# Performance work log

Hardware: AMD Instinct MI355X
Metric: run time of the kernel (lower is better)

Reference implementation:

```python
import jax, jax.numpy as jnp
import numpy as np

N = 100000   # nodes
E = 1600000  # edges (avg degree 16)
DIM = 3      # coordinate dims
R = 3        # pseudo-coordinate dim
C = 32       # channels / Gaussian kernels
F = 64       # non-coordinate node features


def setup_inputs() -> dict:
    key = jax.random.key(0)
    k1, k2, k3, k4, k5 = jax.random.split(key, 5)
    features = jax.random.normal(k1, (N, DIM + F), dtype=jnp.float32)
    edge_index = jax.random.randint(k2, (E, 2), 0, N, dtype=jnp.int32)  # (row=i, col=j) per edge
    w_dense = jax.random.normal(k3, (DIM, R), dtype=jnp.float32) / jnp.sqrt(jnp.float32(DIM))  # lecun-ish
    b_dense = jnp.zeros((R,), dtype=jnp.float32)
    mu = jax.random.normal(k4, (C, N, R), dtype=jnp.float32) * 0.1
    # sigma initialized positive (abs of lecun normal in the original); keep bounded away from 0
    sig = jax.random.uniform(k5, (C, N, R), dtype=jnp.float32, minval=0.1, maxval=1.0)
    return {"features": features, "edge_index": edge_index,
            "w_dense": w_dense, "b_dense": b_dense, "mu": mu, "sig": sig}


def reference(features, edge_index, w_dense, b_dense, mu, sig):
    coords = features[:, :DIM]          # [N, 3]
    h = features[:, DIM:]               # [N, F]
    src = edge_index[:, 0]              # row index i per edge
    dst = edge_index[:, 1]              # col index j per edge
    # per-edge pseudo-coordinates: tanh(Dense_r(x_j - x_i))
    u = jnp.tanh((coords[dst] - coords[src]) @ w_dense + b_dense)      # [E, R]
    # Gaussian-mixture edge weight per (channel, edge), mu/sigma gathered at row node i
    diff = u[None, :, :] - mu[:, src, :]                               # [C, E, R]
    w = jnp.exp(-0.5 * jnp.sum(diff * diff / sig[:, src, :], axis=-1)) # [C, E]
    # (A o W) @ H summed over feature axis == sum_j w[c,i,j] * sum_f H[j,f]
    msg = w * jnp.sum(h, axis=-1)[dst][None, :]                        # [C, E]
    agg = jax.ops.segment_sum(msg.T, src, num_segments=N)              # [N, C]
    return jnp.concatenate([coords, agg], axis=-1)                     # [N, DIM + C]
```

## Files before the change

### kernel.cpp

```cpp
#include <hip/hip_runtime.h>

#define DIMV 3
#define RV 3
#define CV 32
#define ROWF 67
#define ROWO 35
#define CAP 48
#define PADSTR 49
#define SCAN_T 1024
#define NGRP 8
#define BSH 5
#define BNODES 32
#define SEGCAP 192

__device__ __forceinline__ float fast_tanh(float x) {
    float ex = __expf(2.0f * x);
    return (ex - 1.0f) * __builtin_amdgcn_rcpf(ex + 1.0f);
}

__device__ __forceinline__ int xcc_id() {
    int x;
    asm("s_getreg_b32 %0, hwreg(HW_REG_XCC_ID)" : "=s"(x));
    return x & (NGRP - 1);
}

__global__ void prep_kernel(const float* __restrict__ features,
                            float4* __restrict__ nd,
                            int* __restrict__ counts,
                            int* __restrict__ bcur, int nbc,
                            float* __restrict__ out, int N) {
    int gid = blockIdx.x * blockDim.x + threadIdx.x;
    if (gid < N) counts[gid] = 0;
    if (gid < nbc) bcur[gid] = 0;
    int node = gid >> 6;
    int lane = threadIdx.x & 63;
    if (node >= N) return;
    const float* row = features + (size_t)node * ROWF;
    float f0 = row[lane];
    float f1 = (lane < ROWF - 64) ? row[64 + lane] : 0.0f;
    float v = (lane >= DIMV ? f0 : 0.0f) + f1;
    for (int off = 32; off > 0; off >>= 1) v += __shfl_xor(v, off, 64);
    float c0 = __shfl(f0, 0, 64);
    float c1 = __shfl(f0, 1, 64);
    float c2 = __shfl(f0, 2, 64);
    if (lane == 0) nd[node] = make_float4(c0, c1, c2, v);
    if (lane < DIMV) out[(size_t)node * ROWO + lane] = f0;
}

__global__ void bin_kernel(const int2* __restrict__ ei2,
                           int* __restrict__ bcur,
                           unsigned int* __restrict__ bins, int E, int NB) {
    int grp = xcc_id();
    int stride = gridDim.x * blockDim.x;
    for (int e = blockIdx.x * blockDim.x + threadIdx.x; e < E; e += stride) {
        unsigned long long v =
            __builtin_nontemporal_load((const unsigned long long*)ei2 + e);
        int s = (int)(v & 0xffffffffull);
        int d = (int)(v >> 32);
        int b = s >> BSH;
        int g = grp;
        int slot = atomicAdd(bcur + g * NB + b, 1);
#pragma unroll 1
        for (int tries = 0; slot >= SEGCAP && tries < NGRP; ++tries) {
            g = (g + 1) & (NGRP - 1);
            slot = atomicAdd(bcur + g * NB + b, 1);
        }
        if (slot < SEGCAP)
            bins[(size_t)(g * NB + b) * SEGCAP + slot] =
                ((unsigned)(s & (BNODES - 1)) << 17) | (unsigned)d;
    }
}

__global__ __launch_bounds__(256, 6)
void fused_bucket_kernel(const int* __restrict__ bcur,
                         const unsigned int* __restrict__ bins,
                         const float4* __restrict__ nd,
                         const float* __restrict__ wd,
                         const float* __restrict__ bd,
                         const float* __restrict__ mu,
                         const float* __restrict__ sig,
                         float* __restrict__ out, int N, int NB) {
    __shared__ float4 ue[BNODES * PADSTR];
    __shared__ float4 snd[BNODES];
    __shared__ int lcnt[BNODES];
    __shared__ int soff[NGRP + 1];
    int b = blockIdx.x;
    int base = b << BSH;
    int nn = N - base; if (nn > BNODES) nn = BNODES;
    int t = threadIdx.x;
    if (t < BNODES) {
        lcnt[t] = 0;
        snd[t] = (t < nn) ? nd[base + t] : make_float4(0.f, 0.f, 0.f, 0.f);
    }
    if (t < NGRP) {
        int c = bcur[t * NB + b];
        soff[t + 1] = (c > SEGCAP) ? SEGCAP : c;
    }
    if (t == 0) soff[0] = 0;
    __syncthreads();
    if (t == 0) {
#pragma unroll
        for (int g = 0; g < NGRP; ++g) soff[g + 1] += soff[g];
    }
    __syncthreads();
    {
        float w0 = wd[0], w1 = wd[1], w2 = wd[2];
        float w3 = wd[3], w4 = wd[4], w5 = wd[5];
        float w6 = wd[6], w7 = wd[7], w8 = wd[8];
        float b0 = bd[0], b1 = bd[1], b2 = bd[2];
        int total = soff[NGRP];
        for (int r = t; r < total; r += 256) {
            int g = 0;
#pragma unroll
            for (int gg = 1; gg < NGRP; ++gg) if (r >= soff[gg]) g = gg;
            int i = r - soff[g];
            unsigned p = bins[(size_t)(g * NB + b) * SEGCAP + i];
            int sl = p >> 17;
            int d  = p & 0x1FFFF;
            float4 pd = nd[d];
            int k = atomicAdd(&lcnt[sl], 1);
            if (k >= CAP) k = CAP - 1;
            float4 ps = snd[sl];
            float dx = pd.x - ps.x, dy = pd.y - ps.y, dz = pd.z - ps.z;
            float u0 = fast_tanh(dx * w0 + dy * w3 + dz * w6 + b0);
            float u1 = fast_tanh(dx * w1 + dy * w4 + dz * w7 + b1);
            float u2 = fast_tanh(dx * w2 + dy * w5 + dz * w8 + b2);
            ue[sl * PADSTR + (k ^ ((sl >> 3) & 3))] = make_float4(u0, u1, u2, pd.w);
        }
    }
    __syncthreads();
    int wv = t >> 6;
    int l  = t & 63;
    int h  = l >> 5;
    int n  = l & 31;
    size_t slab = (size_t)N * RV;
    int nid = base + ((n < nn) ? n : 0);
    float3 mv[4], sv[4];
#pragma unroll
    for (int j = 0; j < 4; ++j) {
        int c = 8 * wv + 2 * j + h;
        const float* mp = mu  + (size_t)c * slab + (size_t)nid * RV;
        const float* sp = sig + (size_t)c * slab + (size_t)nid * RV;
        mv[j] = *(const float3*)mp;
        sv[j] = *(const float3*)sp;
    }
    float mm[4][3], im[4][3], acc[4];
#pragma unroll
    for (int j = 0; j < 4; ++j) {
        mm[j][0] = mv[j].x; mm[j][1] = mv[j].y; mm[j][2] = mv[j].z;
        im[j][0] = __builtin_amdgcn_rcpf(sv[j].x);
        im[j][1] = __builtin_amdgcn_rcpf(sv[j].y);
        im[j][2] = __builtin_amdgcn_rcpf(sv[j].z);
        acc[j] = 0.0f;
    }
    int cnt = (n < nn) ? min(lcnt[n], CAP) : 0;
    int key = (n >> 3) & 3;
    for (int k = 0; k < cnt; ++k) {
        float4 q = ue[n * PADSTR + (k ^ key)];
#pragma unroll
        for (int j = 0; j < 4; ++j) {
            float d0 = q.x - mm[j][0], d1 = q.y - mm[j][1], d2 = q.z - mm[j][2];
            float t2 = d0 * d0 * im[j][0] + d1 * d1 * im[j][1] + d2 * d2 * im[j][2];
            acc[j] += __expf(-0.5f * t2) * q.w;
        }
    }
    if (n < nn) {
        float* orow = out + (size_t)(base + n) * ROWO + DIMV;
#pragma unroll
        for (int j = 0; j < 4; ++j) orow[8 * wv + 2 * j + h] = acc[j];
    }
}


__global__ void hist_kernel(const int2* __restrict__ ei2, int* __restrict__ counts, int E) {
    int e = blockIdx.x * blockDim.x + threadIdx.x;
    if (e >= E) return;
    atomicAdd(counts + ei2[e].x, 1);
}

__global__ void scan_a_kernel(const int* __restrict__ counts, int* __restrict__ offsets,
                              int* __restrict__ partials, int N) {
    __shared__ int sm[SCAN_T];
    int t = threadIdx.x;
    int i = blockIdx.x * SCAN_T + t;
    int c = (i < N) ? counts[i] : 0;
    sm[t] = c;
    __syncthreads();
    for (int off = 1; off < SCAN_T; off <<= 1) {
        int v = (t >= off) ? sm[t - off] : 0;
        __syncthreads();
        sm[t] += v;
        __syncthreads();
    }
    if (i < N) offsets[i] = sm[t] - c;
    if (t == SCAN_T - 1) partials[blockIdx.x] = sm[t];
}

__global__ void scan_b_kernel(int* __restrict__ partials, int B) {
    __shared__ int sm[SCAN_T];
    int t = threadIdx.x;
    int c = (t < B) ? partials[t] : 0;
    sm[t] = c;
    __syncthreads();
    for (int off = 1; off < SCAN_T; off <<= 1) {
        int v = (t >= off) ? sm[t - off] : 0;
        __syncthreads();
        sm[t] += v;
        __syncthreads();
    }
    if (t < B) partials[t] = sm[t] - c;
}

__global__ void scan_c_kernel(int* __restrict__ offsets, const int* __restrict__ partials,
                              int* __restrict__ cursor, int N, int E) {
    int i = blockIdx.x * blockDim.x + threadIdx.x;
    if (i == 0) offsets[N] = E;
    if (i >= N) return;
    int off = offsets[i] + partials[i / SCAN_T];
    offsets[i] = off;
    cursor[i] = off;
}

__global__ void scatter_u_kernel(const int2* __restrict__ ei2, int* __restrict__ cursor,
                                 const float4* __restrict__ nd,
                                 const float* __restrict__ wd, const float* __restrict__ bd,
                                 float4* __restrict__ ue, int E) {
    int e = blockIdx.x * blockDim.x + threadIdx.x;
    if (e >= E) return;
    int2 sd = ei2[e];
    int pos = atomicAdd(cursor + sd.x, 1);
    float4 ps = nd[sd.x];
    float4 pd = nd[sd.y];
    float dx = pd.x - ps.x, dy = pd.y - ps.y, dz = pd.z - ps.z;
    float u0 = fast_tanh(dx * wd[0] + dy * wd[3] + dz * wd[6] + bd[0]);
    float u1 = fast_tanh(dx * wd[1] + dy * wd[4] + dz * wd[7] + bd[1]);
    float u2 = fast_tanh(dx * wd[2] + dy * wd[5] + dz * wd[8] + bd[2]);
    ue[pos] = make_float4(u0, u1, u2, pd.w);
}

__global__ void node_acc2_kernel(const int* __restrict__ offsets,
                                 const float4* __restrict__ ue,
                                 const float* __restrict__ mu,
                                 const float* __restrict__ sig,
                                 float* __restrict__ out, int N) {
    int node = (blockIdx.x * blockDim.x + threadIdx.x) >> 6;
    if (node >= N) return;
    int lane = threadIdx.x & 63;
    int c = lane & 31;
    int half = lane >> 5;
    size_t slab = (size_t)N * RV;
    const float* mp = mu + (size_t)c * slab + (size_t)node * RV;
    const float* sp = sig + (size_t)c * slab + (size_t)node * RV;
    float m0 = mp[0], m1 = mp[1], m2 = mp[2];
    float i0 = __builtin_amdgcn_rcpf(sp[0]);
    float i1 = __builtin_amdgcn_rcpf(sp[1]);
    float i2 = __builtin_amdgcn_rcpf(sp[2]);
    int off0 = offsets[node], off1 = offsets[node + 1];
    float acc = 0.0f;
    for (int i = off0 + half; i < off1; i += 2) {
        float4 q = ue[i];
        float d0 = q.x - m0, d1 = q.y - m1, d2 = q.z - m2;
        float t = d0 * d0 * i0 + d1 * d1 * i1 + d2 * d2 * i2;
        acc += __expf(-0.5f * t) * q.w;
    }
    acc += __shfl_xor(acc, 32, 64);
    if (half == 0) out[(size_t)node * ROWO + DIMV + c] = acc;
}


__global__ void fb_pre_kernel(const float* __restrict__ features,
                              float4* __restrict__ nd, float* __restrict__ out, int N) {
    int gid = blockIdx.x * blockDim.x + threadIdx.x;
    int node = gid >> 6;
    int lane = threadIdx.x & 63;
    if (node >= N) return;
    const float* row = features + (size_t)node * ROWF;
    float f0 = row[lane];
    float f1 = (lane < ROWF - 64) ? row[64 + lane] : 0.0f;
    float v = (lane >= DIMV ? f0 : 0.0f) + f1;
    for (int off = 32; off > 0; off >>= 1) v += __shfl_xor(v, off, 64);
    float c0 = __shfl(f0, 0, 64);
    float c1 = __shfl(f0, 1, 64);
    float c2 = __shfl(f0, 2, 64);
    if (lane == 0) nd[node] = make_float4(c0, c1, c2, v);
    float* orow = out + (size_t)node * ROWO;
    if (lane < DIMV) orow[lane] = f0;
    else if (lane < ROWO) orow[lane] = 0.0f;
}

__global__ void fb_edge_kernel(const int* __restrict__ ei, const float4* __restrict__ nd,
                               const float* __restrict__ wd, const float* __restrict__ bd,
                               const float* __restrict__ mu, const float* __restrict__ sig,
                               float* __restrict__ out, int N, int E) {
    int e = blockIdx.x * blockDim.x + threadIdx.x;
    if (e >= E) return;
    int s = ei[2 * e];
    int d = ei[2 * e + 1];
    float4 ps = nd[s];
    float4 pd = nd[d];
    float dx = pd.x - ps.x, dy = pd.y - ps.y, dz = pd.z - ps.z;
    float u0 = fast_tanh(dx * wd[0] + dy * wd[3] + dz * wd[6] + bd[0]);
    float u1 = fast_tanh(dx * wd[1] + dy * wd[4] + dz * wd[7] + bd[1]);
    float u2 = fast_tanh(dx * wd[2] + dy * wd[5] + dz * wd[8] + bd[2]);
    float hs = pd.w;
    float* oagg = out + (size_t)s * ROWO + DIMV;
    size_t nodeoff = (size_t)s * RV;
    size_t slab = (size_t)N * RV;
#pragma unroll 4
    for (int c = 0; c < CV; ++c) {
        const float* mp = mu + (size_t)c * slab + nodeoff;
        const float* sp = sig + (size_t)c * slab + nodeoff;
        float d0 = u0 - mp[0], d1 = u1 - mp[1], d2 = u2 - mp[2];
        float t = d0 * d0 * __builtin_amdgcn_rcpf(sp[0])
                + d1 * d1 * __builtin_amdgcn_rcpf(sp[1])
                + d2 * d2 * __builtin_amdgcn_rcpf(sp[2]);
        atomicAdd(oagg + c, __expf(-0.5f * t) * hs);
    }
}

extern "C" void kernel_launch(void* const* d_in, const int* in_sizes, int n_in,
                              void* d_out, int out_size, void* d_ws, size_t ws_size,
                              hipStream_t stream) {
    const float* features = (const float*)d_in[0];
    const int*   ei       = (const int*)d_in[1];
    const int2*  ei2      = (const int2*)d_in[1];
    const float* wd       = (const float*)d_in[2];
    const float* bd       = (const float*)d_in[3];
    const float* mu       = (const float*)d_in[4];
    const float* sig      = (const float*)d_in[5];
    float* out = (float*)d_out;

    int N = in_sizes[0] / ROWF;
    int E = in_sizes[1] / 2;
    int B = (N + SCAN_T - 1) / SCAN_T;
    int NB = (N + BNODES - 1) / BNODES;

    size_t cur = 0;
    auto take = [&](size_t bytes) { size_t p = cur; cur += (bytes + 255) & ~(size_t)255; return p; };
    size_t o_nd      = take((size_t)N * sizeof(float4));
    size_t o_counts  = take((size_t)N * sizeof(int));
    size_t o_offsets = take((size_t)(N + 1) * sizeof(int));
    size_t o_cursor  = take((size_t)N * sizeof(int));
    size_t o_part    = take((size_t)SCAN_T * sizeof(int));
    size_t o_bcur    = take((size_t)NGRP * NB * sizeof(int));
    size_t o_bins    = take((size_t)NGRP * NB * SEGCAP * sizeof(unsigned int));
    size_t o_tail    = cur;
    size_t need_fused = o_tail;
    size_t need_full  = o_tail + (((size_t)E * sizeof(float4) + 255) & ~(size_t)255);

    char* ws = (char*)d_ws;
    float4* nd   = (float4*)(ws + o_nd);
    int* counts  = (int*)(ws + o_counts);
    int* offsets = (int*)(ws + o_offsets);
    int* cursor  = (int*)(ws + o_cursor);
    int* part    = (int*)(ws + o_part);
    int* bcur    = (int*)(ws + o_bcur);
    unsigned int* bins = (unsigned int*)(ws + o_bins);

    if (ws_size >= need_fused && N < (1 << 17)) {
        prep_kernel<<<(N + 3) / 4, 256, 0, stream>>>(features, nd, counts, bcur, NGRP * NB, out, N);
        bin_kernel<<<2048, 256, 0, stream>>>(ei2, bcur, bins, E, NB);
        fused_bucket_kernel<<<NB, 256, 0, stream>>>(bcur, bins, nd, wd, bd, mu, sig, out, N, NB);
    } else if (ws_size >= need_full && B <= SCAN_T) {
        float4* ue = (float4*)(ws + o_tail);
        prep_kernel<<<(N + 3) / 4, 256, 0, stream>>>(features, nd, counts, bcur, 0, out, N);
        hist_kernel<<<(E + 255) / 256, 256, 0, stream>>>(ei2, counts, E);
        scan_a_kernel<<<B, SCAN_T, 0, stream>>>(counts, offsets, part, N);
        scan_b_kernel<<<1, SCAN_T, 0, stream>>>(part, B);
        scan_c_kernel<<<(N + 255) / 256, 256, 0, stream>>>(offsets, part, cursor, N, E);
        scatter_u_kernel<<<(E + 255) / 256, 256, 0, stream>>>(ei2, cursor, nd, wd, bd, ue, E);
        node_acc2_kernel<<<(N + 3) / 4, 256, 0, stream>>>(offsets, ue, mu, sig, out, N);
    } else {
        fb_pre_kernel<<<(N + 3) / 4, 256, 0, stream>>>(features, nd, out, N);
        fb_edge_kernel<<<(E + 255) / 256, 256, 0, stream>>>(ei, nd, wd, bd, mu, sig, out, N, E);
    }
}
```

Before: 256.8 us.

## Replace per-bucket global-atomic binning with LDS-staged coarse partition binning

Edges are now binned into coarse partitions of 1024 source nodes. Each large block stages records in per-partition LDS ring buffers and flushes them in 16-record chunks, using one global atomic per chunk instead of one per edge. Each 32-node bucket block then scans its whole partition with vectorized loads and keeps only the records for its own node group. This cuts global atomic traffic and scattered writes, but every bucket block now reads about 32x more records (mostly from L2) and does a divergent filter. The LDS ring can also overwrite entries if more than 64 edges for one partition arrive in a single pass.

```diff
diff --git a/kernel.cpp b/kernel.cpp
--- a/kernel.cpp
+++ b/kernel.cpp
@@ -8,20 +8,19 @@
 #define CAP 48
 #define PADSTR 49
 #define SCAN_T 1024
-#define NGRP 8
 #define BSH 5
 #define BNODES 32
-#define SEGCAP 192
+#define PART_SH 10
+#define MAXP 128
+#define RING 64
+#define PSEG 24576
+#define CB_BLOCKS 256
+#define CB_THREADS 1024
+#define INVALID_REC 0xFFFFFFFFu
 
 __device__ __forceinline__ float fast_tanh(float x) {
     float ex = __expf(2.0f * x);
     return (ex - 1.0f) * __builtin_amdgcn_rcpf(ex + 1.0f);
-}
-
-__device__ __forceinline__ int xcc_id() {
-    int x;
-    asm("s_getreg_b32 %0, hwreg(HW_REG_XCC_ID)" : "=s"(x));
-    return x & (NGRP - 1);
 }
 
 __global__ void prep_kernel(const float* __restrict__ features,
@@ -47,60 +46,92 @@
     if (lane < DIMV) out[(size_t)node * ROWO + lane] = f0;
 }
 
-__global__ void bin_kernel(const int2* __restrict__ ei2,
-                           int* __restrict__ bcur,
-                           unsigned int* __restrict__ bins, int E, int NB) {
-    int grp = xcc_id();
-    int stride = gridDim.x * blockDim.x;
-    for (int e = blockIdx.x * blockDim.x + threadIdx.x; e < E; e += stride) {
-        unsigned long long v =
-            __builtin_nontemporal_load((const unsigned long long*)ei2 + e);
-        int s = (int)(v & 0xffffffffull);
-        int d = (int)(v >> 32);
-        int b = s >> BSH;
-        int g = grp;
-        int slot = atomicAdd(bcur + g * NB + b, 1);
-#pragma unroll 1
-        for (int tries = 0; slot >= SEGCAP && tries < NGRP; ++tries) {
-            g = (g + 1) & (NGRP - 1);
-            slot = atomicAdd(bcur + g * NB + b, 1);
+__global__ __launch_bounds__(CB_THREADS, 1)
+void coarse_bin_kernel(const int2* __restrict__ ei2,
+                       int* __restrict__ gcur,
+                       unsigned int* __restrict__ bins, int E, int P) {
+    __shared__ unsigned int ring[MAXP][RING];
+    __shared__ int cnt[MAXP];
+    __shared__ int flushed[MAXP];
+    int t = threadIdx.x;
+    for (int i = t; i < P; i += CB_THREADS) { cnt[i] = 0; flushed[i] = 0; }
+    __syncthreads();
+    long long e0 = (long long)E * blockIdx.x / CB_BLOCKS;
+    long long e1 = (long long)E * (blockIdx.x + 1) / CB_BLOCKS;
+    int wv = t >> 6, lane = t & 63;
+    for (long long cs = e0; cs < e1; cs += 2 * CB_THREADS) {
+#pragma unroll
+        for (int j = 0; j < 2; ++j) {
+            long long e = cs + (long long)j * CB_THREADS + t;
+            if (e < e1) {
+                unsigned long long v =
+                    __builtin_nontemporal_load((const unsigned long long*)ei2 + e);
+                int s = (int)(v & 0xffffffffull);
+                int d = (int)(v >> 32);
+                int p = s >> PART_SH;
+                int slot = atomicAdd(&cnt[p], 1);
+                ring[p][slot & (RING - 1)] =
+                    ((unsigned)(s & ((1 << PART_SH) - 1)) << 17) | (unsigned)d;
+            }
         }
-        if (slot < SEGCAP)
-            bins[(size_t)(g * NB + b) * SEGCAP + slot] =
-                ((unsigned)(s & (BNODES - 1)) << 17) | (unsigned)d;
+        __syncthreads();
+        for (int p2 = wv; p2 < P; p2 += CB_THREADS / 64) {
+            int c = cnt[p2];
+            int fl = flushed[p2];
+            int pend = (c >> 4) - fl;
+            while (pend > 0) {
+                int L = pend > 4 ? 4 : pend;
+                int gpos = 0;
+                if (lane == 0) gpos = atomicAdd(&gcur[p2], L << 4);
+                gpos = __shfl(gpos, 0, 64);
+                if (lane < (L << 4) && gpos + (L << 4) <= PSEG)
+                    bins[(size_t)p2 * PSEG + gpos + lane] =
+                        ring[p2][((fl << 4) + lane) & (RING - 1)];
+                fl += L;
+                pend -= L;
+            }
+            if (lane == 0) flushed[p2] = fl;
+        }
+        __syncthreads();
+    }
+    for (int p2 = wv; p2 < P; p2 += CB_THREADS / 64) {
+        int c = cnt[p2];
+        int fl = flushed[p2];
+        int rem = c - (fl << 4);
+        if (rem > 0) {
+            int gpos = 0;
+            if (lane == 0) gpos = atomicAdd(&gcur[p2], 16);
+            gpos = __shfl(gpos, 0, 64);
+            if (lane < 16 && gpos + 16 <= PSEG) {
+                unsigned r = (lane < rem)
+                    ? ring[p2][((fl << 4) + lane) & (RING - 1)] : INVALID_REC;
+                bins[(size_t)p2 * PSEG + gpos + lane] = r;
+            }
+        }
     }
 }
 
 __global__ __launch_bounds__(256, 6)
-void fused_bucket_kernel(const int* __restrict__ bcur,
+void fused_bucket_kernel(const int* __restrict__ gcur,
                          const unsigned int* __restrict__ bins,
                          const float4* __restrict__ nd,
                          const float* __restrict__ wd,
                          const float* __restrict__ bd,
                          const float* __restrict__ mu,
                          const float* __restrict__ sig,
-                         float* __restrict__ out, int N, int NB) {
+                         float* __restrict__ out, int N) {
     __shared__ float4 ue[BNODES * PADSTR];
     __shared__ float4 snd[BNODES];
     __shared__ int lcnt[BNODES];
-    __shared__ int soff[NGRP + 1];
     int b = blockIdx.x;
     int base = b << BSH;
     int nn = N - base; if (nn > BNODES) nn = BNODES;
     int t = threadIdx.x;
+    int p   = b >> (PART_SH - BSH);
+    int grp = b & ((1 << (PART_SH - BSH)) - 1);
     if (t < BNODES) {
         lcnt[t] = 0;
         snd[t] = (t < nn) ? nd[base + t] : make_float4(0.f, 0.f, 0.f, 0.f);
-    }
-    if (t < NGRP) {
-        int c = bcur[t * NB + b];
-        soff[t + 1] = (c > SEGCAP) ? SEGCAP : c;
-    }
-    if (t == 0) soff[0] = 0;
-    __syncthreads();
-    if (t == 0) {
-#pragma unroll
-        for (int g = 0; g < NGRP; ++g) soff[g + 1] += soff[g];
     }
     __syncthreads();
     {
@@ -108,24 +139,32 @@
         float w3 = wd[3], w4 = wd[4], w5 = wd[5];
         float w6 = wd[6], w7 = wd[7], w8 = wd[8];
         float b0 = bd[0], b1 = bd[1], b2 = bd[2];
-        int total = soff[NGRP];
-        for (int r = t; r < total; r += 256) {
-            int g = 0;
-#pragma unroll
-            for (int gg = 1; gg < NGRP; ++gg) if (r >= soff[gg]) g = gg;
-            int i = r - soff[g];
-            unsigned p = bins[(size_t)(g * NB + b) * SEGCAP + i];
-            int sl = p >> 17;
-            int d  = p & 0x1FFFF;
-            float4 pd = nd[d];
-            int k = atomicAdd(&lcnt[sl], 1);
-            if (k >= CAP) k = CAP - 1;
-            float4 ps = snd[sl];
-            float dx = pd.x - ps.x, dy = pd.y - ps.y, dz = pd.z - ps.z;
-            float u0 = fast_tanh(dx * w0 + dy * w3 + dz * w6 + b0);
-            float u1 = fast_tanh(dx * w1 + dy * w4 + dz * w7 + b1);
-            float u2 = fast_tanh(dx * w2 + dy * w5 + dz * w8 + b2);
-            ue[sl * PADSTR + (k ^ ((sl >> 3) & 3))] = make_float4(u0, u1, u2, pd.w);
+        int total = gcur[p];
+        if (total > PSEG) total = PSEG;
+        total &= ~15;
+        const uint4* rp = (const uint4*)(bins + (size_t)p * PSEG);
+        int n4 = total >> 2;
+        for (int i = t; i < n4; i += 256) {
+            uint4 q4 = rp[i];
+            unsigned rr[4] = {q4.x, q4.y, q4.z, q4.w};
+#pragma unroll
+            for (int jj = 0; jj < 4; ++jj) {
+                unsigned r = rr[jj];
+                if ((r >> 22) == (unsigned)grp) {
+                    int sl = (r >> 17) & (BNODES - 1);
+                    int d  = r & 0x1FFFF;
+                    float4 pd = nd[d];
+                    int k = atomicAdd(&lcnt[sl], 1);
+                    if (k >= CAP) k = CAP - 1;
+                    float4 ps = snd[sl];
+                    float dx = pd.x - ps.x, dy = pd.y - ps.y, dz = pd.z - ps.z;
+                    float u0 = fast_tanh(dx * w0 + dy * w3 + dz * w6 + b0);
+                    float u1 = fast_tanh(dx * w1 + dy * w4 + dz * w7 + b1);
+                    float u2 = fast_tanh(dx * w2 + dy * w5 + dz * w8 + b2);
+                    ue[sl * PADSTR + (k ^ ((sl >> 3) & 3))] =
+                        make_float4(u0, u1, u2, pd.w);
+                }
+            }
         }
     }
     __syncthreads();
@@ -334,6 +373,7 @@
     int E = in_sizes[1] / 2;
     int B = (N + SCAN_T - 1) / SCAN_T;
     int NB = (N + BNODES - 1) / BNODES;
+    int P  = (N + (1 << PART_SH) - 1) >> PART_SH;
 
     size_t cur = 0;
     auto take = [&](size_t bytes) { size_t p = cur; cur += (bytes + 255) & ~(size_t)255; return p; };
@@ -342,8 +382,8 @@
     size_t o_offsets = take((size_t)(N + 1) * sizeof(int));
     size_t o_cursor  = take((size_t)N * sizeof(int));
     size_t o_part    = take((size_t)SCAN_T * sizeof(int));
-    size_t o_bcur    = take((size_t)NGRP * NB * sizeof(int));
-    size_t o_bins    = take((size_t)NGRP * NB * SEGCAP * sizeof(unsigned int));
+    size_t o_gcur    = take((size_t)MAXP * sizeof(int));
+    size_t o_bins    = take((size_t)MAXP * PSEG * sizeof(unsigned int));
     size_t o_tail    = cur;
     size_t need_fused = o_tail;
     size_t need_full  = o_tail + (((size_t)E * sizeof(float4) + 255) & ~(size_t)255);
@@ -354,16 +394,16 @@
     int* offsets = (int*)(ws + o_offsets);
     int* cursor  = (int*)(ws + o_cursor);
     int* part    = (int*)(ws + o_part);
-    int* bcur    = (int*)(ws + o_bcur);
+    int* gcur    = (int*)(ws + o_gcur);
     unsigned int* bins = (unsigned int*)(ws + o_bins);
 
     if (ws_size >= need_fused && N < (1 << 17)) {
-        prep_kernel<<<(N + 3) / 4, 256, 0, stream>>>(features, nd, counts, bcur, NGRP * NB, out, N);
-        bin_kernel<<<2048, 256, 0, stream>>>(ei2, bcur, bins, E, NB);
-        fused_bucket_kernel<<<NB, 256, 0, stream>>>(bcur, bins, nd, wd, bd, mu, sig, out, N, NB);
+        prep_kernel<<<(N + 3) / 4, 256, 0, stream>>>(features, nd, counts, gcur, MAXP, out, N);
+        coarse_bin_kernel<<<CB_BLOCKS, CB_THREADS, 0, stream>>>(ei2, gcur, bins, E, P);
+        fused_bucket_kernel<<<NB, 256, 0, stream>>>(gcur, bins, nd, wd, bd, mu, sig, out, N);
     } else if (ws_size >= need_full && B <= SCAN_T) {
         float4* ue = (float4*)(ws + o_tail);
-        prep_kernel<<<(N + 3) / 4, 256, 0, stream>>>(features, nd, counts, bcur, 0, out, N);
+        prep_kernel<<<(N + 3) / 4, 256, 0, stream>>>(features, nd, counts, gcur, 0, out, N);
         hist_kernel<<<(E + 255) / 256, 256, 0, stream>>>(ei2, counts, E);
         scan_a_kernel<<<B, SCAN_T, 0, stream>>>(counts, offsets, part, N);
         scan_b_kernel<<<1, SCAN_T, 0, stream>>>(part, B);
```

After: 623.8 us. 143% more time.
